# Kernel tuning notes

Measured on AMD Instinct MI355X. Metric: run time of the kernel, lower is better.

## Reference

```python
import jax, jax.numpy as jnp
import numpy as np

B, L, D = 4096, 50, 128          # users, neighbors/user, embed_dim
N_U, N_I, N_R, N_T = 10000, 100000, 6, 1000
EPS = 1e-5                       # BatchNorm eps (eval mode, running stats)


def setup_inputs() -> dict:
    key = jax.random.key(0)
    ks = iter(jax.random.split(key, 80))
    nk = lambda: next(ks)

    def lin(din, dout):
        s = 1.0 / np.sqrt(din)
        w = jax.random.uniform(nk(), (din, dout), minval=-s, maxval=s, dtype=jnp.float32)
        b = jax.random.uniform(nk(), (dout,), minval=-s, maxval=s, dtype=jnp.float32)
        return w, b

    inp = {}
    # embedding tables (u2e/i2e/r2e/t2e)
    inp['u2e'] = 0.1 * jax.random.normal(nk(), (N_U, D), jnp.float32)
    inp['i2e'] = 0.1 * jax.random.normal(nk(), (N_I, D), jnp.float32)
    inp['r2e'] = 0.1 * jax.random.normal(nk(), (N_R, D), jnp.float32)
    inp['t2e'] = 0.1 * jax.random.normal(nk(), (N_T, D), jnp.float32)
    # neighbor transform MLP
    inp['ne_w'], inp['ne_b'] = lin(3 * D, D)
    inp['ne1_w'], inp['ne1_b'] = lin(D, D)
    # attention MLP (NewAttention: concat(neigh, user) -> D -> D -> 1, softmax over neighbors)
    inp['att1_w'], inp['att1_b'] = lin(2 * D, D)
    inp['att2_w'], inp['att2_b'] = lin(D, D)
    inp['att3_w'], inp['att3_b'] = lin(D, 1)
    # head
    inp['lin_w'], inp['lin_b'] = lin(2 * D, D)
    inp['w1_w'], inp['w1_b'] = lin(D, D // 4)
    inp['bn1_g'] = jnp.ones((D // 4,), jnp.float32)
    inp['bn1_b'] = jnp.zeros((D // 4,), jnp.float32)
    inp['bn1_m'] = 0.1 * jax.random.normal(nk(), (D // 4,), jnp.float32)
    inp['bn1_v'] = jax.random.uniform(nk(), (D // 4,), minval=0.5, maxval=1.5, dtype=jnp.float32)
    inp['w2_w'], inp['w2_b'] = lin(D // 4, D // 8)
    inp['bn2_g'] = jnp.ones((D // 8,), jnp.float32)
    inp['bn2_b'] = jnp.zeros((D // 8,), jnp.float32)
    inp['bn2_m'] = 0.1 * jax.random.normal(nk(), (D // 8,), jnp.float32)
    inp['bn2_v'] = jax.random.uniform(nk(), (D // 8,), minval=0.5, maxval=1.5, dtype=jnp.float32)
    inp['w3_w'], inp['w3_b'] = lin(D // 8, 1)
    # index inputs (padded-fixed neighbor lists)
    inp['user_idx'] = jax.random.randint(nk(), (B,), 0, N_U)
    inp['item_idx'] = jax.random.randint(nk(), (B, L), 0, N_I)
    inp['rat_idx'] = jax.random.randint(nk(), (B, L), 0, N_R)
    inp['time_idx'] = jax.random.randint(nk(), (B, L), 0, N_T)
    return inp


def reference(u2e, i2e, r2e, t2e, ne_w, ne_b, ne1_w, ne1_b,
              att1_w, att1_b, att2_w, att2_b, att3_w, att3_b,
              lin_w, lin_b, w1_w, w1_b, bn1_g, bn1_b, bn1_m, bn1_v,
              w2_w, w2_b, bn2_g, bn2_b, bn2_m, bn2_v, w3_w, w3_b,
              user_idx, item_idx, rat_idx, time_idx):
    u = u2e[user_idx]                                                   # [B, D]
    neigh = jnp.concatenate([i2e[item_idx], r2e[rat_idx], t2e[time_idx]], axis=-1)  # [B, L, 3D]
    x = jax.nn.relu(neigh @ ne_w + ne_b)                                # [B, L, D]
    x = jax.nn.relu(x @ ne1_w + ne1_b)                                  # [B, L, D]
    # attention over neighbors, conditioned on the user embedding
    a = jnp.concatenate([x, jnp.broadcast_to(u[:, None, :], x.shape)], axis=-1)  # [B, L, 2D]
    a = jax.nn.relu(a @ att1_w + att1_b)
    a = jax.nn.relu(a @ att2_w + att2_b)
    att = jax.nn.softmax((a @ att3_w + att3_b)[..., 0], axis=-1)        # [B, L]
    pooled = jnp.einsum('bl,bld->bd', att, x)                           # torch.mm(x.t(), att).t()
    comb = jax.nn.relu(jnp.concatenate([u, pooled], axis=-1) @ lin_w + lin_b)  # [B, D]
    h = comb @ w1_w + w1_b
    h = jax.nn.relu((h - bn1_m) * jax.lax.rsqrt(bn1_v + EPS) * bn1_g + bn1_b)
    h = h @ w2_w + w2_b
    h = jax.nn.relu((h - bn2_m) * jax.lax.rsqrt(bn2_v + EPS) * bn2_g + bn2_b)
    return (h @ w3_w + w3_b)[:, 0]                                      # [B]
```

## Files before the change

### kernel.cpp

```cpp
#include <hip/hip_runtime.h>
#include <hip/hip_bf16.h>

typedef __bf16 bf16x8 __attribute__((ext_vector_type(8)));
typedef float  f32x4  __attribute__((ext_vector_type(4)));

#define W_OFF 0
#define A_OFF 16384
#define X_OFF 29696
#define SMALL 43008
#define SMEM_TOTAL 47104
#define WCHUNK 16384
#define WHALF  8192

#define WS_WPREP 0
#define WS_PI    262144
#define WS_PT    (WS_PI + 25600000)
#define WS_PR    (WS_PT + 512000)
#define WS_PU    (WS_PR + 3072)
#define WS_PU2   (WS_PU + 5120000)

__global__ void prep_weights_kernel(const float* __restrict__ ne_w,
                                    const float* __restrict__ ne1_w,
                                    const float* __restrict__ att1_w,
                                    const float* __restrict__ att2_w,
                                    const float* __restrict__ lin_w,
                                    __hip_bfloat16* __restrict__ wout) {
  __shared__ float tile[64][65];
  const int bx = blockIdx.x;
  const int c = bx >> 2, kt = (bx >> 1) & 1, ntile = bx & 1;
  const float* src; int koff;
  if      (c < 3)  { src = ne_w;   koff = c * 128; }
  else if (c == 3) { src = ne1_w;  koff = 0; }
  else if (c == 4) { src = att1_w; koff = 0; }
  else if (c == 5) { src = att2_w; koff = 0; }
  else if (c == 6) { src = att1_w; koff = 128; }
  else             { src = lin_w;  koff = 0; }
  const int tx = threadIdx.x, ty = threadIdx.y;
#pragma unroll
  for (int r = 0; r < 16; ++r) {
    int k = kt * 64 + r * 4 + ty, n = ntile * 64 + tx;
    tile[r * 4 + ty][tx] = src[(koff + k) * 128 + n];
  }
  __syncthreads();
#pragma unroll
  for (int r = 0; r < 16; ++r) {
    int n = ntile * 64 + r * 4 + ty, k = kt * 64 + tx;
    int h = k >> 6, k64 = k & 63;
    int off = c * WCHUNK + h * WHALF + n * 64 + ((((k64 >> 3) ^ (n & 7))) << 3) + (k64 & 7);
    wout[off] = __float2bfloat16(tile[tx][r * 4 + ty]);
  }
}

__device__ __forceinline__ unsigned short bf_bits(float x) {
  return __builtin_bit_cast(unsigned short, __float2bfloat16(x));
}

__device__ __forceinline__ void mfma_half(const __hip_bfloat16* sIn,
                                          const __hip_bfloat16* sWh,
                                          f32x4 acc[4], int h, int m16, int nh, int lane) {
  const int mr = lane & 15;
  const int kq = lane >> 4;
  const int arow = (m16 * 16 + mr) * 128;
#pragma unroll
  for (int ks = 0; ks < 2; ++ks) {
    const int kb16 = h * 8 + ks * 4 + kq;
    bf16x8 a = *(const bf16x8*)(sIn + arow + ((kb16 ^ mr) << 3));
    const int swzb = (((ks * 4 + kq) ^ (mr & 7)) << 3);
#pragma unroll
    for (int nt = 0; nt < 4; ++nt) {
      const int n = nh * 64 + nt * 16 + mr;
      bf16x8 b = *(const bf16x8*)(sWh + n * 64 + swzb);
      acc[nt] = __builtin_amdgcn_mfma_f32_16x16x32_bf16(a, b, acc[nt], 0, 0, 0);
    }
  }
}

__device__ __forceinline__ void epilogue(f32x4 acc[4], const float* __restrict__ bias,
                                         const float* addvec, __hip_bfloat16* sOut,
                                         int m16, int nh, int lane) {
  const int mr = lane & 15;
  const int rb = m16 * 16 + ((lane >> 4) << 2);
#pragma unroll
  for (int nt = 0; nt < 4; ++nt) {
    const int col = nh * 64 + nt * 16 + mr;
    float bv = bias[col];
    if (addvec) bv += addvec[col];
    const int cblk = col >> 3, clo = col & 7;
#pragma unroll
    for (int r = 0; r < 4; ++r) {
      const int row = rb + r;
      if (row < 50) {
        float v = fmaxf(acc[nt][r] + bv, 0.0f);
        sOut[row * 128 + ((cblk ^ (row & 15)) << 3) + clo] = __float2bfloat16(v);
      }
    }
  }
}

__global__ __launch_bounds__(512) void pgemm_kernel(
    const float* __restrict__ i2e, const float* __restrict__ r2e,
    const float* __restrict__ t2e, const float* __restrict__ u2e,
    const float* __restrict__ ne_b, const __hip_bfloat16* __restrict__ wprep,
    __hip_bfloat16* __restrict__ Pi, float* __restrict__ Pt, float* __restrict__ Pr,
    float* __restrict__ Pu, float* __restrict__ Pu2) {
  __shared__ __align__(16) __hip_bfloat16 sW[WCHUNK];
  __shared__ __align__(16) __hip_bfloat16 sA[64 * 128];
  const int tid = threadIdx.x, lane = tid & 63, wid = tid >> 6;
  const int m16 = wid & 3, nh = wid >> 2;
  const int bx = blockIdx.x;
  const float* src; const __hip_bfloat16* W; float* dst = nullptr;
  const float* addb = nullptr; bool bf_out = false;
  long rows0; int nrows;
  if (bx < 1563)      { src = i2e; W = wprep + 0 * WCHUNK; bf_out = true; rows0 = (long)bx * 64;          nrows = 100000; }
  else if (bx < 1579) { src = t2e; W = wprep + 2 * WCHUNK; dst = Pt;  rows0 = (long)(bx - 1563) * 64; nrows = 1000; }
  else if (bx < 1580) { src = r2e; W = wprep + 1 * WCHUNK; dst = Pr;  rows0 = 0;                      nrows = 6; addb = ne_b; }
  else if (bx < 1737) { src = u2e; W = wprep + 6 * WCHUNK; dst = Pu;  rows0 = (long)(bx - 1580) * 64; nrows = 10000; }
  else                { src = u2e; W = wprep + 7 * WCHUNK; dst = Pu2; rows0 = (long)(bx - 1737) * 64; nrows = 10000; }

#pragma unroll
  for (int i = 0; i < 4; ++i) {
    int g = tid + i * 512;
    __builtin_amdgcn_global_load_lds(
        (__attribute__((address_space(1))) void*)(void*)(W + g * 8),
        (__attribute__((address_space(3))) void*)(void*)(sW + g * 8), 16, 0, 0);
  }
  const float4* s4 = (const float4*)src;
#pragma unroll
  for (int i = 0; i < 2; ++i) {
    int g = tid + i * 512;
    int row = g >> 4, kb = g & 15;
    float4 v0 = {0.f, 0.f, 0.f, 0.f}, v1 = {0.f, 0.f, 0.f, 0.f};
    if (rows0 + row < nrows) {
      long base = (rows0 + row) * 32 + kb * 2;
      v0 = s4[base]; v1 = s4[base + 1];
    }
    uint4 pk;
    pk.x = ((unsigned)bf_bits(v0.y) << 16) | bf_bits(v0.x);
    pk.y = ((unsigned)bf_bits(v0.w) << 16) | bf_bits(v0.z);
    pk.z = ((unsigned)bf_bits(v1.y) << 16) | bf_bits(v1.x);
    pk.w = ((unsigned)bf_bits(v1.w) << 16) | bf_bits(v1.z);
    *(uint4*)(sA + row * 128 + ((kb ^ (row & 15)) << 3)) = pk;
  }
  __syncthreads();

  f32x4 acc[4];
#pragma unroll
  for (int j = 0; j < 4; ++j) acc[j] = (f32x4){0.f, 0.f, 0.f, 0.f};
  mfma_half(sA, sW, acc, 0, m16, nh, lane);
  mfma_half(sA, sW + WHALF, acc, 1, m16, nh, lane);

  const int mr = lane & 15;
  const int rb = m16 * 16 + ((lane >> 4) << 2);
#pragma unroll
  for (int nt = 0; nt < 4; ++nt) {
    const int col = nh * 64 + nt * 16 + mr;
    const float bv = addb ? addb[col] : 0.f;
#pragma unroll
    for (int r = 0; r < 4; ++r) {
      const int row = rb + r;
      if (rows0 + row < nrows) {
        if (bf_out) Pi[(rows0 + row) * 128 + col] = __float2bfloat16(acc[nt][r]);
        else        dst[(rows0 + row) * 128 + col] = acc[nt][r] + bv;
      }
    }
  }
}

__global__ __launch_bounds__(512, 6) void graphdec_main(
    const __hip_bfloat16* __restrict__ Pi, const float* __restrict__ Pt,
    const float* __restrict__ Pr, const float* __restrict__ Pu,
    const float* __restrict__ Pu2,
    const float* __restrict__ ne1_b, const float* __restrict__ att1_b,
    const float* __restrict__ att2_b, const float* __restrict__ att3_w,
    const float* __restrict__ lin_w, const float* __restrict__ lin_b,
    const float* __restrict__ w1_w, const float* __restrict__ w1_b,
    const float* __restrict__ bn1_g, const float* __restrict__ bn1_b,
    const float* __restrict__ bn1_m, const float* __restrict__ bn1_v,
    const float* __restrict__ w2_w, const float* __restrict__ w2_b,
    const float* __restrict__ bn2_g, const float* __restrict__ bn2_b,
    const float* __restrict__ bn2_m, const float* __restrict__ bn2_v,
    const float* __restrict__ w3_w, const float* __restrict__ w3_b,
    const int* __restrict__ user_idx, const int* __restrict__ item_idx,
    const int* __restrict__ rat_idx, const int* __restrict__ time_idx,
    const __hip_bfloat16* __restrict__ wprep, float* __restrict__ out) {
  __shared__ __align__(16) unsigned char smem[SMEM_TOTAL];
  __hip_bfloat16* sW = (__hip_bfloat16*)(smem + W_OFF);
  __hip_bfloat16* sA = (__hip_bfloat16*)(smem + A_OFF);
  __hip_bfloat16* sX = (__hip_bfloat16*)(smem + X_OFF);
  int*   sIdx   = (int*)  (smem + SMALL);
  float* sUatt  = (float*)(smem + SMALL + 768);
  float* sUlin  = (float*)(smem + SMALL + 1280);
  float* sLP0   = (float*)(smem + SMALL + 1792);
  float* sLP1   = (float*)(smem + SMALL + 2048);
  float* sAtt   = (float*)(smem + SMALL + 2304);
  float* sPooled= (float*)(smem + SMALL + 2560);
  float* sComb  = (float*)(smem + SMALL + 3072);
  float* sH1    = (float*)(smem + SMALL + 3584);
  float* sPool4 = (float*)(smem + W_OFF);
  float* sCombP = (float*)(smem + W_OFF + 2048);

  const int tid  = threadIdx.x;
  const int lane = tid & 63;
  const int wid  = tid >> 6;
  const int m16  = wid & 3;
  const int nh   = wid >> 2;
  const int b    = blockIdx.x;

  float att3r[4];
#pragma unroll
  for (int nt = 0; nt < 4; ++nt) att3r[nt] = att3_w[nh * 64 + nt * 16 + (lane & 15)];

  if (tid < 192) {
    int c = tid >> 6, l = tid & 63;
    int v = 0;
    if (l < 50) {
      const int* p = (c == 0) ? item_idx : (c == 1) ? rat_idx : time_idx;
      v = p[b * 50 + l];
    }
    sIdx[tid] = v;
  }
  const int uid = user_idx[b];
  if (tid >= 256 && tid < 384)      sUatt[tid - 256] = Pu [(long)uid * 128 + (tid - 256)];
  else if (tid >= 384)              sUlin[tid - 384] = Pu2[(long)uid * 128 + (tid - 384)];
  __syncthreads();

  auto stage16 = [&](const __hip_bfloat16* __restrict__ src) {
#pragma unroll
    for (int i = 0; i < 2; ++i) {
      int g = tid + i * 512;
      __builtin_amdgcn_global_load_lds(
          (__attribute__((address_space(1))) void*)(void*)(src + g * 8),
          (__attribute__((address_space(3))) void*)(void*)(sW + g * 8), 16, 0, 0);
    }
  };

  f32x4 acc[4];
  const f32x4 zf = {0.f, 0.f, 0.f, 0.f};
  auto zacc = [&]() {
#pragma unroll
    for (int j = 0; j < 4; ++j) acc[j] = zf;
  };

  stage16(wprep + 3 * WCHUNK);
#pragma unroll
  for (int i = 0; i < 2; ++i) {
    int g = tid + i * 512;
    if (g < 832) {
      int row = g >> 4, kb = g & 15;
      uint4 pk = {0u, 0u, 0u, 0u};
      if (row < 50) {
        const bf16x8 pv = *(const bf16x8*)(Pi + (long)sIdx[row] * 128 + kb * 8);
        const float4* pr4 = (const float4*)(Pr + (long)sIdx[64 + row] * 128) + kb * 2;
        const float4* pt4 = (const float4*)(Pt + (long)sIdx[128 + row] * 128) + kb * 2;
        float4 r0 = pr4[0], r1 = pr4[1];
        float4 t0 = pt4[0], t1 = pt4[1];
        float s0 = fmaxf((float)pv[0] + r0.x + t0.x, 0.f);
        float s1 = fmaxf((float)pv[1] + r0.y + t0.y, 0.f);
        float s2 = fmaxf((float)pv[2] + r0.z + t0.z, 0.f);
        float s3 = fmaxf((float)pv[3] + r0.w + t0.w, 0.f);
        float s4 = fmaxf((float)pv[4] + r1.x + t1.x, 0.f);
        float s5 = fmaxf((float)pv[5] + r1.y + t1.y, 0.f);
        float s6 = fmaxf((float)pv[6] + r1.z + t1.z, 0.f);
        float s7 = fmaxf((float)pv[7] + r1.w + t1.w, 0.f);
        pk.x = ((unsigned)bf_bits(s1) << 16) | bf_bits(s0);
        pk.y = ((unsigned)bf_bits(s3) << 16) | bf_bits(s2);
        pk.z = ((unsigned)bf_bits(s5) << 16) | bf_bits(s4);
        pk.w = ((unsigned)bf_bits(s7) << 16) | bf_bits(s6);
      }
      *(uint4*)(sA + row * 128 + ((kb ^ (row & 15)) << 3)) = pk;
    }
  }
  __syncthreads();

  zacc();
  mfma_half(sA, sW, acc, 0, m16, nh, lane);
  __syncthreads();
  stage16(wprep + 3 * WCHUNK + WHALF);
  __syncthreads();
  mfma_half(sA, sW, acc, 1, m16, nh, lane);
  __syncthreads();
  stage16(wprep + 4 * WCHUNK);
  epilogue(acc, ne1_b, nullptr, sX, m16, nh, lane);
  __syncthreads();

  zacc();
  mfma_half(sX, sW, acc, 0, m16, nh, lane);
  __syncthreads();
  stage16(wprep + 4 * WCHUNK + WHALF);
  __syncthreads();
  mfma_half(sX, sW, acc, 1, m16, nh, lane);
  __syncthreads();
  stage16(wprep + 5 * WCHUNK);
  epilogue(acc, att1_b, sUatt, sA, m16, nh, lane);
  __syncthreads();

  zacc();
  mfma_half(sA, sW, acc, 0, m16, nh, lane);
  __syncthreads();
  stage16(wprep + 5 * WCHUNK + WHALF);
  __syncthreads();
  mfma_half(sA, sW, acc, 1, m16, nh, lane);
  {
    float lp[4] = {0.f, 0.f, 0.f, 0.f};
#pragma unroll
    for (int nt = 0; nt < 4; ++nt) {
      const int col = nh * 64 + nt * 16 + (lane & 15);
      const float b2 = att2_b[col];
#pragma unroll
      for (int r = 0; r < 4; ++r)
        lp[r] += fmaxf(acc[nt][r] + b2, 0.f) * att3r[nt];
    }
#pragma unroll
    for (int off = 1; off < 16; off <<= 1) {
#pragma unroll
      for (int r = 0; r < 4; ++r) lp[r] += __shfl_xor(lp[r], off);
    }
    if ((lane & 15) == 0) {
      const int rowb = m16 * 16 + ((lane >> 4) << 2);
      float* dst = nh ? sLP1 : sLP0;
#pragma unroll
      for (int r = 0; r < 4; ++r) dst[rowb + r] = lp[r];
    }
  }
  __syncthreads();

  if (wid == 0) {
    float v = (lane < 50) ? (sLP0[lane] + sLP1[lane]) : -3.4e38f;
    float m = v;
    for (int off = 32; off > 0; off >>= 1) m = fmaxf(m, __shfl_xor(m, off));
    float e = (lane < 50) ? __expf(v - m) : 0.f;
    float s = e;
    for (int off = 32; off > 0; off >>= 1) s += __shfl_xor(s, off);
    sAtt[lane] = e / s;
  }
  __syncthreads();

  {
    int q = tid >> 7, d = tid & 127;
    const int cblk = d >> 3, clo = d & 7;
    float s = 0.f;
    for (int l = q; l < 50; l += 4)
      s += sAtt[l] * (float)sX[l * 128 + ((cblk ^ (l & 15)) << 3) + clo];
    sPool4[q * 128 + d] = s;
  }
  __syncthreads();
  if (tid < 128)
    sPooled[tid] = sPool4[tid] + sPool4[128 + tid] + sPool4[256 + tid] + sPool4[384 + tid];
  __syncthreads();

  {
    int q = tid >> 7, d = tid & 127;
    float s = 0.f;
    for (int j = q * 32; j < q * 32 + 32; ++j) s += sPooled[j] * lin_w[(128 + j) * 128 + d];
    sCombP[q * 128 + d] = s;
  }
  __syncthreads();
  if (tid < 128)
    sComb[tid] = fmaxf(sCombP[tid] + sCombP[128 + tid] + sCombP[256 + tid] + sCombP[384 + tid]
                       + sUlin[tid] + lin_b[tid], 0.f);
  __syncthreads();

  if (wid == 0) {
    if (lane < 32) {
      float s = w1_b[lane];
      for (int k = 0; k < 128; ++k) s += sComb[k] * w1_w[k * 32 + lane];
      s = (s - bn1_m[lane]) * rsqrtf(bn1_v[lane] + 1e-5f) * bn1_g[lane] + bn1_b[lane];
      sH1[lane] = fmaxf(s, 0.f);
    }
    if (lane < 16) {
      float s = w2_b[lane];
      for (int k = 0; k < 32; ++k) s += sH1[k] * w2_w[k * 16 + lane];
      s = (s - bn2_m[lane]) * rsqrtf(bn2_v[lane] + 1e-5f) * bn2_g[lane] + bn2_b[lane];
      float p = fmaxf(s, 0.f) * w3_w[lane];
      p += __shfl_xor(p, 1); p += __shfl_xor(p, 2);
      p += __shfl_xor(p, 4); p += __shfl_xor(p, 8);
      if (lane == 0) out[b] = p + w3_b[0];
    }
  }
}

extern "C" void kernel_launch(void* const* d_in, const int* in_sizes, int n_in,
                              void* d_out, int out_size, void* d_ws, size_t ws_size,
                              hipStream_t stream) {
  const float* u2e    = (const float*)d_in[0];
  const float* i2e    = (const float*)d_in[1];
  const float* r2e    = (const float*)d_in[2];
  const float* t2e    = (const float*)d_in[3];
  const float* ne_w   = (const float*)d_in[4];
  const float* ne_b   = (const float*)d_in[5];
  const float* ne1_w  = (const float*)d_in[6];
  const float* ne1_b  = (const float*)d_in[7];
  const float* att1_w = (const float*)d_in[8];
  const float* att1_b = (const float*)d_in[9];
  const float* att2_w = (const float*)d_in[10];
  const float* att2_b = (const float*)d_in[11];
  const float* att3_w = (const float*)d_in[12];
  const float* att3_b = (const float*)d_in[13];
  const float* lin_w  = (const float*)d_in[14];
  const float* lin_b  = (const float*)d_in[15];
  const float* w1_w   = (const float*)d_in[16];
  const float* w1_b   = (const float*)d_in[17];
  const float* bn1_g  = (const float*)d_in[18];
  const float* bn1_b  = (const float*)d_in[19];
  const float* bn1_m  = (const float*)d_in[20];
  const float* bn1_v  = (const float*)d_in[21];
  const float* w2_w   = (const float*)d_in[22];
  const float* w2_b   = (const float*)d_in[23];
  const float* bn2_g  = (const float*)d_in[24];
  const float* bn2_b  = (const float*)d_in[25];
  const float* bn2_m  = (const float*)d_in[26];
  const float* bn2_v  = (const float*)d_in[27];
  const float* w3_w   = (const float*)d_in[28];
  const float* w3_b   = (const float*)d_in[29];
  const int* user_idx = (const int*)d_in[30];
  const int* item_idx = (const int*)d_in[31];
  const int* rat_idx  = (const int*)d_in[32];
  const int* time_idx = (const int*)d_in[33];
  (void)att3_b;

  char* ws = (char*)d_ws;
  __hip_bfloat16* wprep = (__hip_bfloat16*)(ws + WS_WPREP);
  __hip_bfloat16* Pi = (__hip_bfloat16*)(ws + WS_PI);
  float* Pt  = (float*)(ws + WS_PT);
  float* Pr  = (float*)(ws + WS_PR);
  float* Pu  = (float*)(ws + WS_PU);
  float* Pu2 = (float*)(ws + WS_PU2);
  float* out = (float*)d_out;

  prep_weights_kernel<<<32, dim3(64, 4), 0, stream>>>(ne_w, ne1_w, att1_w, att2_w,
                                                      lin_w, wprep);
  pgemm_kernel<<<1894, 512, 0, stream>>>(i2e, r2e, t2e, u2e, ne_b, wprep,
                                         Pi, Pt, Pr, Pu, Pu2);
  graphdec_main<<<4096, 512, 0, stream>>>(
      Pi, Pt, Pr, Pu, Pu2, ne1_b, att1_b, att2_b, att3_w,
      lin_w, lin_b, w1_w, w1_b, bn1_g, bn1_b, bn1_m, bn1_v, w2_w, w2_b,
      bn2_g, bn2_b, bn2_m, bn2_v, w3_w, w3_b,
      user_idx, item_idx, rat_idx, time_idx, wprep, out);
}
```

Before: 245.0 us.

## Process two users per block in main kernel and loop row tiles in pgemm

```diff
diff --git a/kernel.cpp b/kernel.cpp
--- a/kernel.cpp
+++ b/kernel.cpp
@@ -6,9 +6,9 @@
 
 #define W_OFF 0
 #define A_OFF 16384
-#define X_OFF 29696
-#define SMALL 43008
-#define SMEM_TOTAL 47104
+#define X_OFF 46080
+#define SMALL 75776
+#define SMEM_TOTAL 80384
 #define WCHUNK 16384
 #define WHALF  8192
 
@@ -55,43 +55,50 @@
   return __builtin_bit_cast(unsigned short, __float2bfloat16(x));
 }
 
-__device__ __forceinline__ void mfma_half(const __hip_bfloat16* sIn,
-                                          const __hip_bfloat16* sWh,
-                                          f32x4 acc[4], int h, int m16, int nh, int lane) {
+__device__ __forceinline__ void mfma_half2(const __hip_bfloat16* sIn,
+                                           const __hip_bfloat16* sWh,
+                                           f32x4 acc[2][4], int h, int m32, int nh,
+                                           int lane) {
   const int mr = lane & 15;
   const int kq = lane >> 4;
-  const int arow = (m16 * 16 + mr) * 128;
 #pragma unroll
   for (int ks = 0; ks < 2; ++ks) {
     const int kb16 = h * 8 + ks * 4 + kq;
-    bf16x8 a = *(const bf16x8*)(sIn + arow + ((kb16 ^ mr) << 3));
+    const int aswz = ((kb16 ^ mr) << 3);
+    bf16x8 a0 = *(const bf16x8*)(sIn + (m32 * 32 + mr) * 128 + aswz);
+    bf16x8 a1 = *(const bf16x8*)(sIn + (m32 * 32 + 16 + mr) * 128 + aswz);
     const int swzb = (((ks * 4 + kq) ^ (mr & 7)) << 3);
 #pragma unroll
     for (int nt = 0; nt < 4; ++nt) {
       const int n = nh * 64 + nt * 16 + mr;
       bf16x8 b = *(const bf16x8*)(sWh + n * 64 + swzb);
-      acc[nt] = __builtin_amdgcn_mfma_f32_16x16x32_bf16(a, b, acc[nt], 0, 0, 0);
-    }
-  }
-}
-
-__device__ __forceinline__ void epilogue(f32x4 acc[4], const float* __restrict__ bias,
-                                         const float* addvec, __hip_bfloat16* sOut,
-                                         int m16, int nh, int lane) {
+      acc[0][nt] = __builtin_amdgcn_mfma_f32_16x16x32_bf16(a0, b, acc[0][nt], 0, 0, 0);
+      acc[1][nt] = __builtin_amdgcn_mfma_f32_16x16x32_bf16(a1, b, acc[1][nt], 0, 0, 0);
+    }
+  }
+}
+
+__device__ __forceinline__ void epilogue2(f32x4 acc[2][4], const float* __restrict__ bias,
+                                          const float* addvec, __hip_bfloat16* sOut,
+                                          int m32, int nh, int lane) {
   const int mr = lane & 15;
-  const int rb = m16 * 16 + ((lane >> 4) << 2);
-#pragma unroll
-  for (int nt = 0; nt < 4; ++nt) {
-    const int col = nh * 64 + nt * 16 + mr;
-    float bv = bias[col];
-    if (addvec) bv += addvec[col];
-    const int cblk = col >> 3, clo = col & 7;
-#pragma unroll
-    for (int r = 0; r < 4; ++r) {
-      const int row = rb + r;
-      if (row < 50) {
-        float v = fmaxf(acc[nt][r] + bv, 0.0f);
-        sOut[row * 128 + ((cblk ^ (row & 15)) << 3) + clo] = __float2bfloat16(v);
+  const int u = m32 >> 1;
+#pragma unroll
+  for (int mt = 0; mt < 2; ++mt) {
+    const int rb = m32 * 32 + mt * 16 + ((lane >> 4) << 2);
+#pragma unroll
+    for (int nt = 0; nt < 4; ++nt) {
+      const int col = nh * 64 + nt * 16 + mr;
+      float bv = bias[col];
+      if (addvec) bv += addvec[u * 128 + col];
+      const int cblk = col >> 3, clo = col & 7;
+#pragma unroll
+      for (int r = 0; r < 4; ++r) {
+        const int row = rb + r;
+        if ((row & 63) < 50) {
+          float v = fmaxf(acc[mt][nt][r] + bv, 0.0f);
+          sOut[row * 128 + ((cblk ^ (row & 15)) << 3) + clo] = __float2bfloat16(v);
+        }
       }
     }
   }
@@ -111,11 +118,11 @@
   const float* src; const __hip_bfloat16* W; float* dst = nullptr;
   const float* addb = nullptr; bool bf_out = false;
   long rows0; int nrows;
-  if (bx < 1563)      { src = i2e; W = wprep + 0 * WCHUNK; bf_out = true; rows0 = (long)bx * 64;          nrows = 100000; }
-  else if (bx < 1579) { src = t2e; W = wprep + 2 * WCHUNK; dst = Pt;  rows0 = (long)(bx - 1563) * 64; nrows = 1000; }
-  else if (bx < 1580) { src = r2e; W = wprep + 1 * WCHUNK; dst = Pr;  rows0 = 0;                      nrows = 6; addb = ne_b; }
-  else if (bx < 1737) { src = u2e; W = wprep + 6 * WCHUNK; dst = Pu;  rows0 = (long)(bx - 1580) * 64; nrows = 10000; }
-  else                { src = u2e; W = wprep + 7 * WCHUNK; dst = Pu2; rows0 = (long)(bx - 1737) * 64; nrows = 10000; }
+  if (bx < 391)      { src = i2e; W = wprep + 0 * WCHUNK; bf_out = true; rows0 = (long)bx * 256;         nrows = 100000; }
+  else if (bx < 395) { src = t2e; W = wprep + 2 * WCHUNK; dst = Pt;  rows0 = (long)(bx - 391) * 256; nrows = 1000; }
+  else if (bx < 396) { src = r2e; W = wprep + 1 * WCHUNK; dst = Pr;  rows0 = 0;                      nrows = 6; addb = ne_b; }
+  else if (bx < 436) { src = u2e; W = wprep + 6 * WCHUNK; dst = Pu;  rows0 = (long)(bx - 396) * 256; nrows = 10000; }
+  else               { src = u2e; W = wprep + 7 * WCHUNK; dst = Pu2; rows0 = (long)(bx - 436) * 256; nrows = 10000; }
 
 #pragma unroll
   for (int i = 0; i < 4; ++i) {
@@ -125,48 +132,69 @@
         (__attribute__((address_space(3))) void*)(void*)(sW + g * 8), 16, 0, 0);
   }
   const float4* s4 = (const float4*)src;
-#pragma unroll
-  for (int i = 0; i < 2; ++i) {
-    int g = tid + i * 512;
-    int row = g >> 4, kb = g & 15;
-    float4 v0 = {0.f, 0.f, 0.f, 0.f}, v1 = {0.f, 0.f, 0.f, 0.f};
-    if (rows0 + row < nrows) {
-      long base = (rows0 + row) * 32 + kb * 2;
-      v0 = s4[base]; v1 = s4[base + 1];
-    }
-    uint4 pk;
-    pk.x = ((unsigned)bf_bits(v0.y) << 16) | bf_bits(v0.x);
-    pk.y = ((unsigned)bf_bits(v0.w) << 16) | bf_bits(v0.z);
-    pk.z = ((unsigned)bf_bits(v1.y) << 16) | bf_bits(v1.x);
-    pk.w = ((unsigned)bf_bits(v1.w) << 16) | bf_bits(v1.z);
-    *(uint4*)(sA + row * 128 + ((kb ^ (row & 15)) << 3)) = pk;
-  }
-  __syncthreads();
-
-  f32x4 acc[4];
-#pragma unroll
-  for (int j = 0; j < 4; ++j) acc[j] = (f32x4){0.f, 0.f, 0.f, 0.f};
-  mfma_half(sA, sW, acc, 0, m16, nh, lane);
-  mfma_half(sA, sW + WHALF, acc, 1, m16, nh, lane);
-
   const int mr = lane & 15;
   const int rb = m16 * 16 + ((lane >> 4) << 2);
-#pragma unroll
-  for (int nt = 0; nt < 4; ++nt) {
-    const int col = nh * 64 + nt * 16 + mr;
-    const float bv = addb ? addb[col] : 0.f;
-#pragma unroll
-    for (int r = 0; r < 4; ++r) {
-      const int row = rb + r;
-      if (rows0 + row < nrows) {
-        if (bf_out) Pi[(rows0 + row) * 128 + col] = __float2bfloat16(acc[nt][r]);
-        else        dst[(rows0 + row) * 128 + col] = acc[nt][r] + bv;
-      }
-    }
-  }
-}
-
-__global__ __launch_bounds__(512, 6) void graphdec_main(
+
+  for (int t = 0; t < 4; ++t) {
+    const long r0 = rows0 + t * 64;
+#pragma unroll
+    for (int i = 0; i < 2; ++i) {
+      int g = tid + i * 512;
+      int row = g >> 4, kb = g & 15;
+      float4 v0 = {0.f, 0.f, 0.f, 0.f}, v1 = {0.f, 0.f, 0.f, 0.f};
+      if (r0 + row < nrows) {
+        long base = (r0 + row) * 32 + kb * 2;
+        v0 = s4[base]; v1 = s4[base + 1];
+      }
+      uint4 pk;
+      pk.x = ((unsigned)bf_bits(v0.y) << 16) | bf_bits(v0.x);
+      pk.y = ((unsigned)bf_bits(v0.w) << 16) | bf_bits(v0.z);
+      pk.z = ((unsigned)bf_bits(v1.y) << 16) | bf_bits(v1.x);
+      pk.w = ((unsigned)bf_bits(v1.w) << 16) | bf_bits(v1.z);
+      *(uint4*)(sA + row * 128 + ((kb ^ (row & 15)) << 3)) = pk;
+    }
+    __syncthreads();
+
+    f32x4 acc[4];
+#pragma unroll
+    for (int j = 0; j < 4; ++j) acc[j] = (f32x4){0.f, 0.f, 0.f, 0.f};
+    {
+      const int kq = lane >> 4;
+#pragma unroll
+      for (int h = 0; h < 2; ++h) {
+        const __hip_bfloat16* sWh = sW + h * WHALF;
+#pragma unroll
+        for (int ks = 0; ks < 2; ++ks) {
+          const int kb16 = h * 8 + ks * 4 + kq;
+          bf16x8 a = *(const bf16x8*)(sA + (m16 * 16 + mr) * 128 + ((kb16 ^ mr) << 3));
+          const int swzb = (((ks * 4 + kq) ^ (mr & 7)) << 3);
+#pragma unroll
+          for (int nt = 0; nt < 4; ++nt) {
+            const int n = nh * 64 + nt * 16 + mr;
+            bf16x8 b = *(const bf16x8*)(sWh + n * 64 + swzb);
+            acc[nt] = __builtin_amdgcn_mfma_f32_16x16x32_bf16(a, b, acc[nt], 0, 0, 0);
+          }
+        }
+      }
+    }
+#pragma unroll
+    for (int nt = 0; nt < 4; ++nt) {
+      const int col = nh * 64 + nt * 16 + mr;
+      const float bv = addb ? addb[col] : 0.f;
+#pragma unroll
+      for (int r = 0; r < 4; ++r) {
+        const int row = rb + r;
+        if (r0 + row < nrows) {
+          if (bf_out) Pi[(r0 + row) * 128 + col] = __float2bfloat16(acc[nt][r]);
+          else        dst[(r0 + row) * 128 + col] = acc[nt][r] + bv;
+        }
+      }
+    }
+    __syncthreads();
+  }
+}
+
+__global__ __launch_bounds__(512, 4) void graphdec_main(
     const __hip_bfloat16* __restrict__ Pi, const float* __restrict__ Pt,
     const float* __restrict__ Pr, const float* __restrict__ Pu,
     const float* __restrict__ Pu2,
@@ -188,21 +216,21 @@
   __hip_bfloat16* sA = (__hip_bfloat16*)(smem + A_OFF);
   __hip_bfloat16* sX = (__hip_bfloat16*)(smem + X_OFF);
   int*   sIdx   = (int*)  (smem + SMALL);
-  float* sUatt  = (float*)(smem + SMALL + 768);
-  float* sUlin  = (float*)(smem + SMALL + 1280);
-  float* sLP0   = (float*)(smem + SMALL + 1792);
-  float* sLP1   = (float*)(smem + SMALL + 2048);
-  float* sAtt   = (float*)(smem + SMALL + 2304);
-  float* sPooled= (float*)(smem + SMALL + 2560);
-  float* sComb  = (float*)(smem + SMALL + 3072);
-  float* sH1    = (float*)(smem + SMALL + 3584);
+  float* sUatt  = (float*)(smem + SMALL + 1536);
+  float* sUlin  = (float*)(smem + SMALL + 2560);
+  float* sLP0   = (float*)(smem + SMALL + 3584);
+  float* sLP1   = (float*)(smem + SMALL + 4096);
   float* sPool4 = (float*)(smem + W_OFF);
   float* sCombP = (float*)(smem + W_OFF + 2048);
+  float* sAtt   = (float*)(smem + W_OFF + 4096);
+  float* sPooled= (float*)(smem + W_OFF + 4608);
+  float* sComb  = (float*)(smem + W_OFF + 5632);
+  float* sH1    = (float*)(smem + W_OFF + 6656);
 
   const int tid  = threadIdx.x;
   const int lane = tid & 63;
   const int wid  = tid >> 6;
-  const int m16  = wid & 3;
+  const int m32  = wid & 3;
   const int nh   = wid >> 2;
   const int b    = blockIdx.x;
 
@@ -210,18 +238,21 @@
 #pragma unroll
   for (int nt = 0; nt < 4; ++nt) att3r[nt] = att3_w[nh * 64 + nt * 16 + (lane & 15)];
 
-  if (tid < 192) {
-    int c = tid >> 6, l = tid & 63;
+  if (tid < 384) {
+    int c = tid >> 7, rest = tid & 127, u = rest >> 6, l = rest & 63;
     int v = 0;
     if (l < 50) {
       const int* p = (c == 0) ? item_idx : (c == 1) ? rat_idx : time_idx;
-      v = p[b * 50 + l];
+      v = p[(2 * b + u) * 50 + l];
     }
     sIdx[tid] = v;
   }
-  const int uid = user_idx[b];
-  if (tid >= 256 && tid < 384)      sUatt[tid - 256] = Pu [(long)uid * 128 + (tid - 256)];
-  else if (tid >= 384)              sUlin[tid - 384] = Pu2[(long)uid * 128 + (tid - 384)];
+  {
+    int u = tid >> 8, r = tid & 255;
+    const long uidu = user_idx[2 * b + u];
+    if (r < 128) sUatt[u * 128 + r]         = Pu [uidu * 128 + r];
+    else         sUlin[u * 128 + (r - 128)] = Pu2[uidu * 128 + (r - 128)];
+  }
   __syncthreads();
 
   auto stage16 = [&](const __hip_bfloat16* __restrict__ src) {
@@ -234,24 +265,28 @@
     }
   };
 
-  f32x4 acc[4];
+  f32x4 acc[2][4];
   const f32x4 zf = {0.f, 0.f, 0.f, 0.f};
   auto zacc = [&]() {
 #pragma unroll
-    for (int j = 0; j < 4; ++j) acc[j] = zf;
+    for (int i = 0; i < 2; ++i)
+#pragma unroll
+      for (int j = 0; j < 4; ++j) acc[i][j] = zf;
   };
 
   stage16(wprep + 3 * WCHUNK);
 #pragma unroll
-  for (int i = 0; i < 2; ++i) {
+  for (int i = 0; i < 4; ++i) {
     int g = tid + i * 512;
-    if (g < 832) {
-      int row = g >> 4, kb = g & 15;
+    if (g < 1664) {
+      int u = (g >= 832) ? 1 : 0;
+      int gl = g - u * 832;
+      int l = gl >> 4, kb = gl & 15;
       uint4 pk = {0u, 0u, 0u, 0u};
-      if (row < 50) {
-        const bf16x8 pv = *(const bf16x8*)(Pi + (long)sIdx[row] * 128 + kb * 8);
-        const float4* pr4 = (const float4*)(Pr + (long)sIdx[64 + row] * 128) + kb * 2;
-        const float4* pt4 = (const float4*)(Pt + (long)sIdx[128 + row] * 128) + kb * 2;
+      if (l < 50) {
+        const bf16x8 pv = *(const bf16x8*)(Pi + (long)sIdx[u * 64 + l] * 128 + kb * 8);
+        const float4* pr4 = (const float4*)(Pr + (long)sIdx[128 + u * 64 + l] * 128) + kb * 2;
+        const float4* pt4 = (const float4*)(Pt + (long)sIdx[256 + u * 64 + l] * 128) + kb * 2;
         float4 r0 = pr4[0], r1 = pr4[1];
         float4 t0 = pt4[0], t1 = pt4[1];
         float s0 = fmaxf((float)pv[0] + r0.x + t0.x, 0.f);
@@ -267,114 +302,131 @@
         pk.z = ((unsigned)bf_bits(s5) << 16) | bf_bits(s4);
         pk.w = ((unsigned)bf_bits(s7) << 16) | bf_bits(s6);
       }
+      const int row = u * 64 + l;
       *(uint4*)(sA + row * 128 + ((kb ^ (row & 15)) << 3)) = pk;
     }
   }
   __syncthreads();
 
   zacc();
-  mfma_half(sA, sW, acc, 0, m16, nh, lane);
+  mfma_half2(sA, sW, acc, 0, m32, nh, lane);
   __syncthreads();
   stage16(wprep + 3 * WCHUNK + WHALF);
   __syncthreads();
-  mfma_half(sA, sW, acc, 1, m16, nh, lane);
+  mfma_half2(sA, sW, acc, 1, m32, nh, lane);
   __syncthreads();
   stage16(wprep + 4 * WCHUNK);
-  epilogue(acc, ne1_b, nullptr, sX, m16, nh, lane);
+  epilogue2(acc, ne1_b, nullptr, sX, m32, nh, lane);
   __syncthreads();
 
   zacc();
-  mfma_half(sX, sW, acc, 0, m16, nh, lane);
+  mfma_half2(sX, sW, acc, 0, m32, nh, lane);
   __syncthreads();
   stage16(wprep + 4 * WCHUNK + WHALF);
   __syncthreads();
-  mfma_half(sX, sW, acc, 1, m16, nh, lane);
+  mfma_half2(sX, sW, acc, 1, m32, nh, lane);
   __syncthreads();
   stage16(wprep + 5 * WCHUNK);
-  epilogue(acc, att1_b, sUatt, sA, m16, nh, lane);
+  epilogue2(acc, att1_b, sUatt, sA, m32, nh, lane);
   __syncthreads();
 
   zacc();
-  mfma_half(sA, sW, acc, 0, m16, nh, lane);
+  mfma_half2(sA, sW, acc, 0, m32, nh, lane);
   __syncthreads();
   stage16(wprep + 5 * WCHUNK + WHALF);
   __syncthreads();
-  mfma_half(sA, sW, acc, 1, m16, nh, lane);
+  mfma_half2(sA, sW, acc, 1, m32, nh, lane);
   {
-    float lp[4] = {0.f, 0.f, 0.f, 0.f};
+    float lp[2][4] = {{0.f, 0.f, 0.f, 0.f}, {0.f, 0.f, 0.f, 0.f}};
 #pragma unroll
     for (int nt = 0; nt < 4; ++nt) {
       const int col = nh * 64 + nt * 16 + (lane & 15);
       const float b2 = att2_b[col];
 #pragma unroll
-      for (int r = 0; r < 4; ++r)
-        lp[r] += fmaxf(acc[nt][r] + b2, 0.f) * att3r[nt];
+      for (int mt = 0; mt < 2; ++mt)
+#pragma unroll
+        for (int r = 0; r < 4; ++r)
+          lp[mt][r] += fmaxf(acc[mt][nt][r] + b2, 0.f) * att3r[nt];
     }
 #pragma unroll
     for (int off = 1; off < 16; off <<= 1) {
 #pragma unroll
-      for (int r = 0; r < 4; ++r) lp[r] += __shfl_xor(lp[r], off);
+      for (int mt = 0; mt < 2; ++mt)
+#pragma unroll
+        for (int r = 0; r < 4; ++r) lp[mt][r] += __shfl_xor(lp[mt][r], off);
     }
     if ((lane & 15) == 0) {
-      const int rowb = m16 * 16 + ((lane >> 4) << 2);
       float* dst = nh ? sLP1 : sLP0;
 #pragma unroll
-      for (int r = 0; r < 4; ++r) dst[rowb + r] = lp[r];
-    }
-  }
-  __syncthreads();
-
-  if (wid == 0) {
-    float v = (lane < 50) ? (sLP0[lane] + sLP1[lane]) : -3.4e38f;
+      for (int mt = 0; mt < 2; ++mt) {
+        const int rowb = m32 * 32 + mt * 16 + ((lane >> 4) << 2);
+#pragma unroll
+        for (int r = 0; r < 4; ++r) dst[rowb + r] = lp[mt][r];
+      }
+    }
+  }
+  __syncthreads();
+
+  if (wid < 2) {
+    const int u = wid;
+    float v = (lane < 50) ? (sLP0[u * 64 + lane] + sLP1[u * 64 + lane]) : -3.4e38f;
     float m = v;
     for (int off = 32; off > 0; off >>= 1) m = fmaxf(m, __shfl_xor(m, off));
     float e = (lane < 50) ? __expf(v - m) : 0.f;
     float s = e;
     for (int off = 32; off > 0; off >>= 1) s += __shfl_xor(s, off);
-    sAtt[lane] = e / s;
+    sAtt[u * 64 + lane] = e / s;
   }
   __syncthreads();
 
   {
-    int q = tid >> 7, d = tid & 127;
+    int u = tid >> 8, q = (tid >> 7) & 1, d = tid & 127;
     const int cblk = d >> 3, clo = d & 7;
     float s = 0.f;
-    for (int l = q; l < 50; l += 4)
-      s += sAtt[l] * (float)sX[l * 128 + ((cblk ^ (l & 15)) << 3) + clo];
-    sPool4[q * 128 + d] = s;
-  }
-  __syncthreads();
-  if (tid < 128)
-    sPooled[tid] = sPool4[tid] + sPool4[128 + tid] + sPool4[256 + tid] + sPool4[384 + tid];
+    for (int l = q; l < 50; l += 2) {
+      const int row = u * 64 + l;
+      s += sAtt[row] * (float)sX[row * 128 + ((cblk ^ (row & 15)) << 3) + clo];
+    }
+    sPool4[(u * 2 + q) * 128 + d] = s;
+  }
+  __syncthreads();
+  if (tid < 256) {
+    int u = tid >> 7, d = tid & 127;
+    sPooled[u * 128 + d] = sPool4[(u * 2) * 128 + d] + sPool4[(u * 2 + 1) * 128 + d];
+  }
   __syncthreads();
 
   {
-    int q = tid >> 7, d = tid & 127;
+    int u = tid >> 8, q = (tid >> 7) & 1, d = tid & 127;
     float s = 0.f;
-    for (int j = q * 32; j < q * 32 + 32; ++j) s += sPooled[j] * lin_w[(128 + j) * 128 + d];
-    sCombP[q * 128 + d] = s;
-  }
-  __syncthreads();
-  if (tid < 128)
-    sComb[tid] = fmaxf(sCombP[tid] + sCombP[128 + tid] + sCombP[256 + tid] + sCombP[384 + tid]
-                       + sUlin[tid] + lin_b[tid], 0.f);
-  __syncthreads();
-
-  if (wid == 0) {
+    for (int j = q * 64; j < q * 64 + 64; ++j)
+      s += sPooled[u * 128 + j] * lin_w[(128 + j) * 128 + d];
+    sCombP[(u * 2 + q) * 128 + d] = s;
+  }
+  __syncthreads();
+  if (tid < 256) {
+    int u = tid >> 7, d = tid & 127;
+    sComb[u * 128 + d] = fmaxf(sCombP[(u * 2) * 128 + d] + sCombP[(u * 2 + 1) * 128 + d]
+                               + sUlin[u * 128 + d] + lin_b[d], 0.f);
+  }
+  __syncthreads();
+
+  if (wid < 2) {
+    const int u = wid;
     if (lane < 32) {
       float s = w1_b[lane];
-      for (int k = 0; k < 128; ++k) s += sComb[k] * w1_w[k * 32 + lane];
+      for (int k = 0; k < 128; ++k) s += sComb[u * 128 + k] * w1_w[k * 32 + lane];
       s = (s - bn1_m[lane]) * rsqrtf(bn1_v[lane] + 1e-5f) * bn1_g[lane] + bn1_b[lane];
-      sH1[lane] = fmaxf(s, 0.f);
+      sH1[u * 32 + lane] = fmaxf(s, 0.f);
     }
     if (lane < 16) {
       float s = w2_b[lane];
-      for (int k = 0; k < 32; ++k) s += sH1[k] * w2_w[k * 16 + lane];
+      for (int k = 0; k < 32; ++k) s += sH1[u * 32 + k] * w2_w[k * 16 + lane];
       s = (s - bn2_m[lane]) * rsqrtf(bn2_v[lane] + 1e-5f) * bn2_g[lane] + bn2_b[lane];
       float p = fmaxf(s, 0.f) * w3_w[lane];
       p += __shfl_xor(p, 1); p += __shfl_xor(p, 2);
       p += __shfl_xor(p, 4); p += __shfl_xor(p, 8);
-      if (lane == 0) out[b] = p + w3_b[0];
+      if (lane == 0) out[2 * b + u] = p + w3_b[0];
     }
   }
 }
@@ -429,9 +481,9 @@
 
   prep_weights_kernel<<<32, dim3(64, 4), 0, stream>>>(ne_w, ne1_w, att1_w, att2_w,
                                                       lin_w, wprep);
-  pgemm_kernel<<<1894, 512, 0, stream>>>(i2e, r2e, t2e, u2e, ne_b, wprep,
-                                         Pi, Pt, Pr, Pu, Pu2);
-  graphdec_main<<<4096, 512, 0, stream>>>(
+  pgemm_kernel<<<476, 512, 0, stream>>>(i2e, r2e, t2e, u2e, ne_b, wprep,
+                                        Pi, Pt, Pr, Pu, Pu2);
+  graphdec_main<<<2048, 512, 0, stream>>>(
       Pi, Pt, Pr, Pu, Pu2, ne1_b, att1_b, att2_b, att3_w,
       lin_w, lin_b, w1_w, w1_b, bn1_g, bn1_b, bn1_m, bn1_v, w2_w, w2_b,
       bn2_g, bn2_b, bn2_m, bn2_v, w3_w, w3_b,
```

New measurement: 246.9 us. No clear change (+0.7%).
